# Performance work log

Hardware: AMD Instinct MI355X
Metric: run time of the kernel (lower is better)

## Reference

```python
import jax, jax.numpy as jnp
import numpy as np

EMBED_DIM = 1024
NUM_HEADS = 8                      # diff-attn heads; effective standard heads = 2*NUM_HEADS
HEAD_DIM = EMBED_DIM // NUM_HEADS // 2   # 64
DEPTH = 12
LAMBDA_INIT = 0.8 - 0.6 * float(np.exp(-0.3 * DEPTH))
RMS_EPS = 1e-5


def _rope_interleaved(x, cos, sin):
    # x: [B,S,H,D]; cos,sin: [S,D//2]. GPT-J style: rotate (even, odd) pairs.
    x1, x2 = x[..., ::2], x[..., 1::2]
    c = cos[None, :, None, :]
    s = sin[None, :, None, :]
    o1 = x1 * c - x2 * s
    o2 = x1 * s + x2 * c
    return jnp.stack([o1, o2], axis=-1).reshape(x.shape)


def _causal_attn(q, k, v, scale):
    # q,k: [B,S,H,D]; v: [B,S,H,Dv] -> out [B,S,H,Dv]
    S = q.shape[1]
    scores = jnp.einsum('bqhd,bkhd->bhqk', q, k) * scale
    causal = jnp.tril(jnp.ones((S, S), dtype=bool))
    scores = jnp.where(causal[None, None], scores, jnp.finfo(scores.dtype).min)
    p = jax.nn.softmax(scores, axis=-1)
    return jnp.einsum('bhqk,bkhd->bqhd', p, v)


def setup_inputs() -> dict:
    key = jax.random.key(0)
    ks = jax.random.split(key, 10)
    B, S, E, D = 1, 2048, EMBED_DIM, HEAD_DIM
    x = jax.random.normal(ks[0], (B, S, E), jnp.float32)
    # real rotary tables, rotary_dim = head_dim = 64 -> cos/sin [S, 32]
    inv_freq = 1.0 / (10000.0 ** (np.arange(0, D, 2, dtype=np.float64) / D))
    freqs = np.outer(np.arange(S, dtype=np.float64), inv_freq)
    cos = jnp.asarray(np.cos(freqs), jnp.float32)
    sin = jnp.asarray(np.sin(freqs), jnp.float32)
    sc = 1.0 / np.sqrt(E)
    wq = jax.random.normal(ks[1], (E, E), jnp.float32) * sc
    wk = jax.random.normal(ks[2], (E, E), jnp.float32) * sc
    wv = jax.random.normal(ks[3], (E, E), jnp.float32) * sc
    wo = jax.random.normal(ks[4], (E, E), jnp.float32) * sc
    lambda_q1 = jax.random.normal(ks[5], (D,), jnp.float32) * 0.1
    lambda_k1 = jax.random.normal(ks[6], (D,), jnp.float32) * 0.1
    lambda_q2 = jax.random.normal(ks[7], (D,), jnp.float32) * 0.1
    lambda_k2 = jax.random.normal(ks[8], (D,), jnp.float32) * 0.1
    subln_weight = jnp.ones((2 * D,), jnp.float32)
    return dict(x=x, cos=cos, sin=sin, wq=wq, wk=wk, wv=wv, wo=wo,
                lambda_q1=lambda_q1, lambda_k1=lambda_k1,
                lambda_q2=lambda_q2, lambda_k2=lambda_k2,
                subln_weight=subln_weight)


def reference(x, cos, sin, wq, wk, wv, wo,
              lambda_q1, lambda_k1, lambda_q2, lambda_k2, subln_weight):
    B, S, E = x.shape
    H, D = NUM_HEADS, HEAD_DIM
    q = (x @ wq).reshape(B, S, 2 * H, D)
    k = (x @ wk).reshape(B, S, 2 * H, D)
    v = (x @ wv).reshape(B, S, H, 2 * D)
    q = _rope_interleaved(q, cos, sin)
    k = _rope_interleaved(k, cos, sin)
    q = q.reshape(B, S, H, 2, D)
    k = k.reshape(B, S, H, 2, D)
    q1, q2 = q[..., 0, :], q[..., 1, :]
    k1, k2 = k[..., 0, :], k[..., 1, :]
    scale = D ** -0.5  # flash_attn default softmax scale
    a1 = _causal_attn(q1, k1, v, scale)  # [B,S,H,2D]
    a2 = _causal_attn(q2, k2, v, scale)
    lam1 = jnp.exp(jnp.sum(lambda_q1 * lambda_k1))
    lam2 = jnp.exp(jnp.sum(lambda_q2 * lambda_k2))
    lam_full = lam1 - lam2 + LAMBDA_INIT
    attn = a1 - lam_full * a2
    # sublayer RMSNorm over 2*head_dim, computed in fp32
    ms = jnp.mean(jnp.square(attn.astype(jnp.float32)), axis=-1, keepdims=True)
    attn = (attn.astype(jnp.float32) * jax.lax.rsqrt(ms + RMS_EPS)).astype(attn.dtype)
    attn = attn * subln_weight
    attn = attn * (1.0 - LAMBDA_INIT)
    attn = attn.reshape(B, S, E)
    return attn @ wo
```

## Files before the change

kernel.cpp:

```cpp
#include <hip/hip_runtime.h>
#include <hip/hip_bf16.h>

#define SEQ 2048
#define EMB 1024
#define NH 8
#define HD 64
#define DVH 128
#define LAMBDA_INIT 0.7836057665316245f
#define ONE_MINUS_LI 0.2163942334683755f
#define RMS_EPS 1e-5f
#define QK_SCALE 0.18033688011112042f

typedef __attribute__((ext_vector_type(8))) short short8_t;
typedef __attribute__((ext_vector_type(4))) float f32x4;

__device__ __forceinline__ short f2bf(float f) {
    __hip_bfloat16 h = __float2bfloat16(f);
    return *reinterpret_cast<short*>(&h);
}
__device__ __forceinline__ float bf2f(short s) {
    unsigned u = ((unsigned)(unsigned short)s) << 16;
    return __uint_as_float(u);
}
__device__ __forceinline__ float fast_exp2(float x) {
    float r;
    asm("v_exp_f32 %0, %1" : "=v"(r) : "v"(x));
    return r;
}
__device__ __forceinline__ void gload16(const void* g, void* l) {
    __builtin_amdgcn_global_load_lds((const __attribute__((address_space(1))) unsigned int*)g,
                                     (__attribute__((address_space(3))) unsigned int*)l, 16, 0, 0);
}

__global__ __launch_bounds__(256) void k_prep(const float* __restrict__ x, short* __restrict__ xb,
                                              const float* __restrict__ w0, const float* __restrict__ w1,
                                              const float* __restrict__ w2, const float* __restrict__ w3,
                                              short* __restrict__ o0, short* __restrict__ o1,
                                              short* __restrict__ o2, short* __restrict__ o3,
                                              const float* __restrict__ lq1, const float* __restrict__ lk1,
                                              const float* __restrict__ lq2, const float* __restrict__ lk2,
                                              float* __restrict__ lam) {
    const int bid = blockIdx.x;
    const int tid = threadIdx.x;
    if (bid < 2048) {
        int i = bid * 256 + tid;
        const float4* xv = (const float4*)x;
        float4 v = xv[i];
        short4 r = make_short4(f2bf(v.x), f2bf(v.y), f2bf(v.z), f2bf(v.w));
        *(short4*)(xb + i * 4) = r;
    } else if (bid < 3072) {
        int t = bid - 2048;
        int bz = t >> 8, by = (t >> 4) & 15, bx = t & 15;
        const float* w = bz == 0 ? w0 : bz == 1 ? w1 : bz == 2 ? w2 : w3;
        short* o = bz == 0 ? o0 : bz == 1 ? o1 : bz == 2 ? o2 : o3;
        __shared__ float tbuf[64][65];
        int r0 = by * 64, c0 = bx * 64;
        int col = tid & 63, rb = tid >> 6;
#pragma unroll
        for (int i = 0; i < 16; i++) {
            int row = rb + i * 4;
            tbuf[row][col] = w[(r0 + row) * EMB + c0 + col];
        }
        __syncthreads();
#pragma unroll
        for (int i = 0; i < 16; i++) {
            int fr = rb + i * 4;
            o[(c0 + fr) * EMB + r0 + col] = f2bf(tbuf[col][fr]);
        }
    } else {
        if (tid < 64) {
            float p1 = lq1[tid] * lk1[tid], p2 = lq2[tid] * lk2[tid];
#pragma unroll
            for (int off = 32; off >= 1; off >>= 1) {
                p1 += __shfl_xor(p1, off);
                p2 += __shfl_xor(p2, off);
            }
            if (tid == 0) lam[0] = expf(p1) - expf(p2) + LAMBDA_INIT;
        }
    }
}

template <int MI, int NI, int OUTM>
__global__ __launch_bounds__(256) void k_gemm(const short* __restrict__ A,
                                              const short* __restrict__ B0,
                                              const short* __restrict__ B1,
                                              const short* __restrict__ B2,
                                              const float* __restrict__ cosT,
                                              const float* __restrict__ sinT,
                                              short* __restrict__ Cq, short* __restrict__ Ktl,
                                              short* __restrict__ Vtl, float* __restrict__ Cf) {
    constexpr int BM = MI * 32, BN = NI * 32, BK = 64;
    constexpr int STAGE_SZ = (BM + BN) * BK;
    constexpr int SH_EPI = (OUTM == 0) ? BM * 136 : 0;
    constexpr int SHSZ = (2 * STAGE_SZ > SH_EPI) ? 2 * STAGE_SZ : SH_EPI;
    __shared__ short SH[SHSZ];
    const int bn = blockIdx.x * BN;
    const int bm = blockIdx.y * BM;
    const int nsel = bn >> 10;
    const int nloc = bn & 1023;
    const short* Bt = nsel == 0 ? B0 : (nsel == 1 ? B1 : B2);
    const int tid = threadIdx.x;
    const int w = tid >> 6, l = tid & 63;
    const int lr = l & 15, lg = l >> 4;
    const int wm = (w >> 1) * (MI * 16), wn = (w & 1) * (NI * 16);
    const int lrow8 = l >> 3, lchunk = l & 7;
    const int schunk = (lchunk ^ lrow8) * 8;

    f32x4 acc[MI][NI];
#pragma unroll
    for (int mi = 0; mi < MI; mi++)
#pragma unroll
        for (int ni = 0; ni < NI; ni++) acc[mi][ni] = f32x4{0.f, 0.f, 0.f, 0.f};

#define STAGEIT(BUF, K0)                                                                      \
    {                                                                                         \
        short* Ab_ = SH + (BUF) * STAGE_SZ;                                                   \
        short* Bb_ = Ab_ + BM * BK;                                                           \
        _Pragma("unroll") for (int j = 0; j < BM / 32; j++) {                                 \
            int r0 = w * (BM / 4) + j * 8;                                                    \
            gload16(A + (size_t)(bm + r0 + lrow8) * EMB + (K0) + schunk, &Ab_[r0 * BK]);      \
        }                                                                                     \
        _Pragma("unroll") for (int j = 0; j < BN / 32; j++) {                                 \
            int r0 = w * (BN / 4) + j * 8;                                                    \
            gload16(Bt + (size_t)(nloc + r0 + lrow8) * EMB + (K0) + schunk, &Bb_[r0 * BK]);   \
        }                                                                                     \
    }

    STAGEIT(0, 0);
    __syncthreads();
#pragma unroll 1
    for (int t = 0; t < EMB / BK; ++t) {
        const int cur = t & 1;
        if (t + 1 < EMB / BK) STAGEIT(cur ^ 1, (t + 1) * BK);
        const short* Ab_ = SH + cur * STAGE_SZ;
        const short* Bb_ = Ab_ + BM * BK;
#pragma unroll
        for (int kk = 0; kk < 2; kk++) {
            const int pcs = (((kk << 2) + lg) ^ (lr & 7)) << 3;
            short8_t af[MI], bf[NI];
#pragma unroll
            for (int mi = 0; mi < MI; mi++)
                af[mi] = *(const short8_t*)&Ab_[(wm + mi * 16 + lr) * BK + pcs];
#pragma unroll
            for (int ni = 0; ni < NI; ni++)
                bf[ni] = *(const short8_t*)&Bb_[(wn + ni * 16 + lr) * BK + pcs];
#pragma unroll
            for (int mi = 0; mi < MI; mi++)
#pragma unroll
                for (int ni = 0; ni < NI; ni++)
                    acc[mi][ni] =
                        __builtin_amdgcn_mfma_f32_16x16x32_bf16(af[mi], bf[ni], acc[mi][ni], 0, 0, 0);
        }
        __syncthreads();
    }
#undef STAGEIT

    if (OUTM == 1) {
#pragma unroll
        for (int mi = 0; mi < MI; mi++)
#pragma unroll
            for (int ni = 0; ni < NI; ni++)
#pragma unroll
                for (int r = 0; r < 4; r++) {
                    int row = bm + wm + mi * 16 + lg * 4 + r;
                    int col = wn + ni * 16 + lr;
                    Cf[row * EMB + bn + col] = acc[mi][ni][r];
                }
        return;
    }
    const int hh = nloc >> 7;
    short* tile = SH;
    if (nsel < 2) {
#pragma unroll
        for (int mi = 0; mi < MI; mi++)
#pragma unroll
            for (int ni = 0; ni < NI; ni++) {
                const int c = wn + ni * 16 + lr;
                const int p = (c & 63) >> 1;
#pragma unroll
                for (int r = 0; r < 4; r++) {
                    const int row = wm + mi * 16 + lg * 4 + r;
                    const int grow = bm + row;
                    float v = acc[mi][ni][r];
                    float partner = __shfl_xor(v, 1);
                    float cs = cosT[grow * 32 + p], sn = sinT[grow * 32 + p];
                    float out = (lr & 1) ? (partner * sn + v * cs) : (v * cs - partner * sn);
                    if (nsel == 0)
                        Cq[((size_t)hh << 18) + (size_t)grow * 128 + c] = f2bf(out * QK_SCALE);
                    else
                        tile[row * 136 + c] = f2bf(out);
                }
            }
        if (nsel == 1) {
            __syncthreads();
            const int kb0 = blockIdx.y * (BM / 32);
#pragma unroll
            for (int i = 0; i < BM / 16; i++) {
                int flat = tid + i * 256;
                int kbi = flat >> 9, rest = flat & 511;
                int slot = rest >> 6, ln = rest & 63;
                int lqq = ln & 15;
                int comp = slot >> 2, tt = (slot >> 1) & 1, s = slot & 1;
                int lgg = ln >> 4;
                int row = kbi * 32 + tt * 16 + lqq;
                int fb = comp * 64 + s * 32 + lgg * 8;
                short8_t v = *(const short8_t*)&tile[row * 136 + fb];
                *(short8_t*)(Ktl + ((size_t)(hh * 64 + kb0 + kbi) * 8 + slot) * 512 + ln * 8) = v;
            }
        }
    } else {
#pragma unroll
        for (int mi = 0; mi < MI; mi++)
#pragma unroll
            for (int ni = 0; ni < NI; ni++) {
                const int c = wn + ni * 16 + lr;
#pragma unroll
                for (int r = 0; r < 4; r++) {
                    const int row = wm + mi * 16 + lg * 4 + r;
                    tile[row * 136 + c] = f2bf(acc[mi][ni][r]);
                }
            }
        __syncthreads();
        const int kb0 = blockIdx.y * (BM / 32);
#pragma unroll
        for (int i = 0; i < BM / 16; i++) {
            int flat = tid + i * 256;
            int kbi = flat >> 9, rest = flat & 511;
            int dt = rest >> 6, ln = rest & 63;
            int lgg = ln >> 4, lqq = ln & 15;
            short8_t v;
#pragma unroll
            for (int j = 0; j < 8; j++)
                v[j] = tile[(kbi * 32 + 16 * (j >> 2) + 4 * lgg + (j & 3)) * 136 + dt * 16 + lqq];
            *(short8_t*)(Vtl + ((size_t)(hh * 64 + kb0 + kbi) * 8 + dt) * 512 + ln * 8) = v;
        }
    }
}

__global__ __launch_bounds__(512, 2) void k_attn(const short* __restrict__ Qh,
                                                 const short* __restrict__ Ktl,
                                                 const short* __restrict__ Vtl,
                                                 const float* __restrict__ lamp,
                                                 const float* __restrict__ subln,
                                                 short* __restrict__ Ab) {
    const int bid = blockIdx.x;
    const int h = bid & 7;
    const int ta = bid >> 3;
    const int tb = 63 - ta;
    const int q0a = ta * 32, q0b = tb * 32;
    const int nba = ta + 1, nbb = tb + 1;
    const int tid = threadIdx.x;
    const int w = tid >> 6, l = tid & 63;
    const int lq = l & 15, lg = l >> 4;
    const int comp = w >> 2, ks = w & 3;

    __shared__ __align__(16) float buf[2][2][16][132];
    __shared__ float LBp[2][4][16];

    short8_t qa0[2], qa1[2], qb0[2], qb1[2];
    {
        const short* qpa = Qh + ((size_t)h << 18) + (size_t)(q0a + lq) * 128 + (comp << 6) + lg * 8;
        qa0[0] = *(const short8_t*)(qpa);
        qa0[1] = *(const short8_t*)(qpa + 32);
        qa1[0] = *(const short8_t*)(qpa + 16 * 128);
        qa1[1] = *(const short8_t*)(qpa + 16 * 128 + 32);
        const short* qpb = Qh + ((size_t)h << 18) + (size_t)(q0b + lq) * 128 + (comp << 6) + lg * 8;
        qb0[0] = *(const short8_t*)(qpb);
        qb0[1] = *(const short8_t*)(qpb + 32);
        qb1[0] = *(const short8_t*)(qpb + 16 * 128);
        qb1[1] = *(const short8_t*)(qpb + 16 * 128 + 32);
    }
    f32x4 zero4 = {0.f, 0.f, 0.f, 0.f};
    f32x4 oa0[8], oa1[8], ob0[8], ob1[8];
#pragma unroll
    for (int dt = 0; dt < 8; dt++) {
        oa0[dt] = zero4;
        oa1[dt] = zero4;
        ob0[dt] = zero4;
        ob1[dt] = zero4;
    }
    float lsa0 = 0.f, lsa1 = 0.f, lsb0 = 0.f, lsb1 = 0.f;

    short8_t vf[8];
    short8_t kf[2][2];

#define PROC1(O, LS, QF, QROW, K0P)                                                          \
    {                                                                                        \
        f32x4 s_[2];                                                                         \
        s_[0] = zero4;                                                                       \
        s_[0] = __builtin_amdgcn_mfma_f32_16x16x32_bf16(kf[0][0], QF[0], s_[0], 0, 0, 0);    \
        s_[0] = __builtin_amdgcn_mfma_f32_16x16x32_bf16(kf[0][1], QF[1], s_[0], 0, 0, 0);    \
        s_[1] = zero4;                                                                       \
        s_[1] = __builtin_amdgcn_mfma_f32_16x16x32_bf16(kf[1][0], QF[0], s_[1], 0, 0, 0);    \
        s_[1] = __builtin_amdgcn_mfma_f32_16x16x32_bf16(kf[1][1], QF[1], s_[1], 0, 0, 0);    \
        float p_[8];                                                                         \
        _Pragma("unroll") for (int tt = 0; tt < 2; tt++)                                     \
            _Pragma("unroll") for (int r = 0; r < 4; r++) p_[tt * 4 + r] = s_[tt][r];        \
        if ((K0P) + 31 > (QROW)) {                                                           \
            _Pragma("unroll") for (int tt = 0; tt < 2; tt++)                                 \
                _Pragma("unroll") for (int r = 0; r < 4; r++) {                              \
                    int kk = (K0P) + tt * 16 + lg * 4 + r;                                   \
                    if (kk > (QROW) + lq) p_[tt * 4 + r] = -1e30f;                           \
                }                                                                            \
        }                                                                                    \
        _Pragma("unroll") for (int i = 0; i < 8; i++) {                                      \
            p_[i] = fast_exp2(p_[i]);                                                        \
            LS += p_[i];                                                                     \
        }                                                                                    \
        unsigned pu_[4];                                                                     \
        _Pragma("unroll") for (int pr = 0; pr < 4; pr++) {                                   \
            float2 f_ = {p_[2 * pr], p_[2 * pr + 1]};                                        \
            __hip_bfloat162 h_ = __float22bfloat162_rn(f_);                                  \
            __builtin_memcpy(&pu_[pr], &h_, 4);                                              \
        }                                                                                    \
        short8_t pa_;                                                                        \
        __builtin_memcpy(&pa_, pu_, 16);                                                     \
        _Pragma("unroll") for (int dt = 0; dt < 8; dt++)                                     \
            O[dt] = __builtin_amdgcn_mfma_f32_16x16x32_bf16(pa_, vf[dt], O[dt], 0, 0, 0);    \
    }

#pragma unroll 1
    for (int kb = ks; kb < nbb; kb += 4) {
        const int k0p = kb * 32;
        {
            const short* vtb = Vtl + (size_t)(h * 64 + kb) * 4096 + l * 8;
            const short* ktb = Ktl + ((size_t)(h * 64 + kb) * 8 + comp * 4) * 512 + l * 8;
#pragma unroll
            for (int dt = 0; dt < 8; dt++) vf[dt] = *(const short8_t*)(vtb + dt * 512);
#pragma unroll
            for (int tt = 0; tt < 2; tt++) {
                kf[tt][0] = *(const short8_t*)(ktb + (tt * 2) * 512);
                kf[tt][1] = *(const short8_t*)(ktb + (tt * 2 + 1) * 512);
            }
        }
        PROC1(ob0, lsb0, qb0, q0b, k0p);
        PROC1(ob1, lsb1, qb1, q0b + 16, k0p);
        if (kb < nba) {
            PROC1(oa0, lsa0, qa0, q0a, k0p);
            PROC1(oa1, lsa1, qa1, q0a + 16, k0p);
        }
    }
#undef PROC1

    lsa0 += __shfl_xor(lsa0, 16);
    lsa0 += __shfl_xor(lsa0, 32);
    lsa1 += __shfl_xor(lsa1, 16);
    lsa1 += __shfl_xor(lsa1, 32);
    lsb0 += __shfl_xor(lsb0, 16);
    lsb0 += __shfl_xor(lsb0, 32);
    lsb1 += __shfl_xor(lsb1, 16);
    lsb1 += __shfl_xor(lsb1, 32);

#define MERGE(O, LS, QBASE)                                                                  \
    {                                                                                        \
        if (ks >= 2) {                                                                       \
            _Pragma("unroll") for (int dt = 0; dt < 8; dt++)                                 \
                _Pragma("unroll") for (int r = 0; r < 4; r++)                                \
                    buf[comp][ks - 2][lg * 4 + r][dt * 16 + lq] = O[dt][r];                  \
            if (l < 16) LBp[comp][ks][l] = LS;                                               \
        }                                                                                    \
        __syncthreads();                                                                     \
        f32x4 oacc_[8];                                                                      \
        float lacc_ = LS;                                                                    \
        if (ks < 2) {                                                                        \
            _Pragma("unroll") for (int dt = 0; dt < 8; dt++)                                 \
                _Pragma("unroll") for (int r = 0; r < 4; r++)                                \
                    oacc_[dt][r] = O[dt][r] + buf[comp][ks][lg * 4 + r][dt * 16 + lq];       \
            lacc_ = LS + LBp[comp][ks + 2][lq];                                              \
        }                                                                                    \
        __syncthreads();                                                                     \
        if (ks == 1) {                                                                       \
            _Pragma("unroll") for (int dt = 0; dt < 8; dt++)                                 \
                _Pragma("unroll") for (int r = 0; r < 4; r++)                                \
                    buf[comp][0][lg * 4 + r][dt * 16 + lq] = oacc_[dt][r];                   \
            if (l < 16) LBp[comp][1][l] = lacc_;                                             \
        }                                                                                    \
        __syncthreads();                                                                     \
        if (ks == 0) {                                                                       \
            _Pragma("unroll") for (int dt = 0; dt < 8; dt++)                                 \
                _Pragma("unroll") for (int r = 0; r < 4; r++)                                \
                    oacc_[dt][r] += buf[comp][0][lg * 4 + r][dt * 16 + lq];                  \
            lacc_ += LBp[comp][1][lq];                                                       \
            const float cs_ = comp ? lamp[0] : 1.f;                                         \
            float inv_[4];                                                                   \
            _Pragma("unroll") for (int r = 0; r < 4; r++)                                    \
                inv_[r] = cs_ / __shfl(lacc_, lg * 4 + r);                                   \
            _Pragma("unroll") for (int dt = 0; dt < 8; dt++)                                 \
                _Pragma("unroll") for (int r = 0; r < 4; r++)                                \
                    buf[comp][1][lg * 4 + r][dt * 16 + lq] = oacc_[dt][r] * inv_[r];         \
        }                                                                                    \
        __syncthreads();                                                                     \
        if (tid < 128) {                                                                     \
            const int row_ = tid >> 3;                                                       \
            const int c0_ = (tid & 7) * 16;                                                  \
            float a_[16], ss_ = 0.f;                                                         \
            _Pragma("unroll") for (int j = 0; j < 16; j++) {                                 \
                a_[j] = buf[0][1][row_][c0_ + j] - buf[1][1][row_][c0_ + j];                 \
                ss_ += a_[j] * a_[j];                                                        \
            }                                                                                \
            ss_ += __shfl_xor(ss_, 1);                                                       \
            ss_ += __shfl_xor(ss_, 2);                                                       \
            ss_ += __shfl_xor(ss_, 4);                                                       \
            const float sc_ = rsqrtf(ss_ * (1.0f / 128.0f) + RMS_EPS) * ONE_MINUS_LI;        \
            short8_t r8_;                                                                    \
            _Pragma("unroll") for (int j = 0; j < 8; j++)                                    \
                r8_[j] = f2bf(a_[j] * sc_ * subln[c0_ + j]);                                 \
            *(short8_t*)(Ab + (size_t)((QBASE) + row_) * EMB + h * DVH + c0_) = r8_;         \
            _Pragma("unroll") for (int j = 0; j < 8; j++)                                    \
                r8_[j] = f2bf(a_[8 + j] * sc_ * subln[c0_ + 8 + j]);                         \
            *(short8_t*)(Ab + (size_t)((QBASE) + row_) * EMB + h * DVH + c0_ + 8) = r8_;     \
        }                                                                                    \
        __syncthreads();                                                                     \
    }

    MERGE(ob0, lsb0, q0b);
    MERGE(ob1, lsb1, q0b + 16);
    MERGE(oa0, lsa0, q0a);
    MERGE(oa1, lsa1, q0a + 16);
#undef MERGE
}

extern "C" void kernel_launch(void* const* d_in, const int* in_sizes, int n_in,
                              void* d_out, int out_size, void* d_ws, size_t ws_size,
                              hipStream_t stream) {
    const float* x = (const float*)d_in[0];
    const float* cosT = (const float*)d_in[1];
    const float* sinT = (const float*)d_in[2];
    const float* wq = (const float*)d_in[3];
    const float* wk = (const float*)d_in[4];
    const float* wv = (const float*)d_in[5];
    const float* wo = (const float*)d_in[6];
    const float* lq1 = (const float*)d_in[7];
    const float* lk1 = (const float*)d_in[8];
    const float* lq2 = (const float*)d_in[9];
    const float* lk2 = (const float*)d_in[10];
    const float* subln = (const float*)d_in[11];
    float* out = (float*)d_out;
    char* ws = (char*)d_ws;
    const size_t MB = 1 << 20;
    short* xb = (short*)(ws);
    short* wqt = (short*)(ws + 4 * MB);
    short* wkt = (short*)(ws + 6 * MB);
    short* wvt = (short*)(ws + 8 * MB);
    short* wot = (short*)(ws + 10 * MB);
    short* Qh = (short*)(ws + 12 * MB);
    short* Vtl = (short*)(ws + 20 * MB);
    short* Ktl = (short*)(ws + 24 * MB);
    short* Ab = (short*)(ws + 28 * MB);
    float* lam = (float*)(ws + 32 * MB);

    k_prep<<<3073, 256, 0, stream>>>(x, xb, wq, wk, wv, wo, wqt, wkt, wvt, wot, lq1, lk1, lq2,
                                     lk2, lam);
    k_gemm<2, 4, 0><<<dim3(24, 32), 256, 0, stream>>>(xb, wqt, wkt, wvt, cosT, sinT, Qh, Ktl,
                                                      Vtl, nullptr);
    k_attn<<<256, 512, 0, stream>>>(Qh, Ktl, Vtl, lam, subln, Ab);
    k_gemm<2, 2, 1><<<dim3(16, 32), 256, 0, stream>>>(Ab, wot, wot, wot, nullptr, nullptr,
                                                      nullptr, nullptr, nullptr, out);
}
```

Baseline: 77.58 us.

## Halve attention block to two K-split waves and double-buffer K/V loads

The attention kernel drops from 8 waves (4-way key split per component) to 4 waves (2-way split), each wave walking its key blocks with ping-pong register buffers so the next block's K/V loads are issued before the current block's MFMAs. The cross-wave merge shrinks from a two-stage reduction with three barriers to a single store/sync/add. In exchange, each block has half the waves to hide latency, more registers per thread (launch bounds 256,1), and each wave does twice the serial work per block.

```diff
diff --git a/kernel.cpp b/kernel.cpp
--- a/kernel.cpp
+++ b/kernel.cpp
@@ -237,7 +237,7 @@
     }
 }
 
-__global__ __launch_bounds__(512, 2) void k_attn(const short* __restrict__ Qh,
+__global__ __launch_bounds__(256, 1) void k_attn(const short* __restrict__ Qh,
                                                  const short* __restrict__ Ktl,
                                                  const short* __restrict__ Vtl,
                                                  const float* __restrict__ lamp,
@@ -252,10 +252,10 @@
     const int tid = threadIdx.x;
     const int w = tid >> 6, l = tid & 63;
     const int lq = l & 15, lg = l >> 4;
-    const int comp = w >> 2, ks = w & 3;
+    const int comp = w >> 1, ks = w & 1;
 
     __shared__ __align__(16) float buf[2][2][16][132];
-    __shared__ float LBp[2][4][16];
+    __shared__ float LBp[2][16];
 
     short8_t qa0[2], qa1[2], qb0[2], qb1[2];
     {
@@ -281,18 +281,30 @@
     }
     float lsa0 = 0.f, lsa1 = 0.f, lsb0 = 0.f, lsb1 = 0.f;
 
-    short8_t vf[8];
-    short8_t kf[2][2];
-
-#define PROC1(O, LS, QF, QROW, K0P)                                                          \
+    short8_t vfA[8], vfB[8];
+    short8_t kfA[2][2], kfB[2][2];
+
+#define LOADKV(VF, KF, KB)                                                                  \
+    {                                                                                       \
+        const short* vtb = Vtl + (size_t)(h * 64 + (KB)) * 4096 + l * 8;                    \
+        const short* ktb = Ktl + ((size_t)(h * 64 + (KB)) * 8 + comp * 4) * 512 + l * 8;    \
+        _Pragma("unroll") for (int dt = 0; dt < 8; dt++) VF[dt] =                           \
+            *(const short8_t*)(vtb + dt * 512);                                             \
+        _Pragma("unroll") for (int tt = 0; tt < 2; tt++) {                                  \
+            KF[tt][0] = *(const short8_t*)(ktb + (tt * 2) * 512);                           \
+            KF[tt][1] = *(const short8_t*)(ktb + (tt * 2 + 1) * 512);                       \
+        }                                                                                   \
+    }
+
+#define PROC1(O, LS, QF, QROW, K0P, KF, VF)                                                  \
     {                                                                                        \
         f32x4 s_[2];                                                                         \
         s_[0] = zero4;                                                                       \
-        s_[0] = __builtin_amdgcn_mfma_f32_16x16x32_bf16(kf[0][0], QF[0], s_[0], 0, 0, 0);    \
-        s_[0] = __builtin_amdgcn_mfma_f32_16x16x32_bf16(kf[0][1], QF[1], s_[0], 0, 0, 0);    \
+        s_[0] = __builtin_amdgcn_mfma_f32_16x16x32_bf16(KF[0][0], QF[0], s_[0], 0, 0, 0);    \
+        s_[0] = __builtin_amdgcn_mfma_f32_16x16x32_bf16(KF[0][1], QF[1], s_[0], 0, 0, 0);    \
         s_[1] = zero4;                                                                       \
-        s_[1] = __builtin_amdgcn_mfma_f32_16x16x32_bf16(kf[1][0], QF[0], s_[1], 0, 0, 0);    \
-        s_[1] = __builtin_amdgcn_mfma_f32_16x16x32_bf16(kf[1][1], QF[1], s_[1], 0, 0, 0);    \
+        s_[1] = __builtin_amdgcn_mfma_f32_16x16x32_bf16(KF[1][0], QF[0], s_[1], 0, 0, 0);    \
+        s_[1] = __builtin_amdgcn_mfma_f32_16x16x32_bf16(KF[1][1], QF[1], s_[1], 0, 0, 0);    \
         float p_[8];                                                                         \
         _Pragma("unroll") for (int tt = 0; tt < 2; tt++)                                     \
             _Pragma("unroll") for (int r = 0; r < 4; r++) p_[tt * 4 + r] = s_[tt][r];        \
@@ -316,31 +328,34 @@
         short8_t pa_;                                                                        \
         __builtin_memcpy(&pa_, pu_, 16);                                                     \
         _Pragma("unroll") for (int dt = 0; dt < 8; dt++)                                     \
-            O[dt] = __builtin_amdgcn_mfma_f32_16x16x32_bf16(pa_, vf[dt], O[dt], 0, 0, 0);    \
-    }
-
+            O[dt] = __builtin_amdgcn_mfma_f32_16x16x32_bf16(pa_, VF[dt], O[dt], 0, 0, 0);    \
+    }
+
+#define PROC4(KF, VF, KB)                                                                    \
+    {                                                                                        \
+        const int k0p_ = (KB) * 32;                                                          \
+        PROC1(ob0, lsb0, qb0, q0b, k0p_, KF, VF);                                            \
+        PROC1(ob1, lsb1, qb1, q0b + 16, k0p_, KF, VF);                                       \
+        if ((KB) < nba) {                                                                    \
+            PROC1(oa0, lsa0, qa0, q0a, k0p_, KF, VF);                                        \
+            PROC1(oa1, lsa1, qa1, q0a + 16, k0p_, KF, VF);                                   \
+        }                                                                                    \
+    }
+
+    LOADKV(vfA, kfA, ks);
 #pragma unroll 1
     for (int kb = ks; kb < nbb; kb += 4) {
-        const int k0p = kb * 32;
-        {
-            const short* vtb = Vtl + (size_t)(h * 64 + kb) * 4096 + l * 8;
-            const short* ktb = Ktl + ((size_t)(h * 64 + kb) * 8 + comp * 4) * 512 + l * 8;
-#pragma unroll
-            for (int dt = 0; dt < 8; dt++) vf[dt] = *(const short8_t*)(vtb + dt * 512);
-#pragma unroll
-            for (int tt = 0; tt < 2; tt++) {
-                kf[tt][0] = *(const short8_t*)(ktb + (tt * 2) * 512);
-                kf[tt][1] = *(const short8_t*)(ktb + (tt * 2 + 1) * 512);
-            }
-        }
-        PROC1(ob0, lsb0, qb0, q0b, k0p);
-        PROC1(ob1, lsb1, qb1, q0b + 16, k0p);
-        if (kb < nba) {
-            PROC1(oa0, lsa0, qa0, q0a, k0p);
-            PROC1(oa1, lsa1, qa1, q0a + 16, k0p);
-        }
-    }
+        const bool hb = (kb + 2) < nbb;
+        if (hb) LOADKV(vfB, kfB, kb + 2);
+        PROC4(kfA, vfA, kb);
+        if (hb) {
+            if (kb + 4 < nbb) LOADKV(vfA, kfA, kb + 4);
+            PROC4(kfB, vfB, kb + 2);
+        }
+    }
+#undef PROC4
 #undef PROC1
+#undef LOADKV
 
     lsa0 += __shfl_xor(lsa0, 16);
     lsa0 += __shfl_xor(lsa0, 32);
@@ -353,35 +368,20 @@
 
 #define MERGE(O, LS, QBASE)                                                                  \
     {                                                                                        \
-        if (ks >= 2) {                                                                       \
-            _Pragma("unroll") for (int dt = 0; dt < 8; dt++)                                 \
-                _Pragma("unroll") for (int r = 0; r < 4; r++)                                \
-                    buf[comp][ks - 2][lg * 4 + r][dt * 16 + lq] = O[dt][r];                  \
-            if (l < 16) LBp[comp][ks][l] = LS;                                               \
-        }                                                                                    \
-        __syncthreads();                                                                     \
-        f32x4 oacc_[8];                                                                      \
-        float lacc_ = LS;                                                                    \
-        if (ks < 2) {                                                                        \
-            _Pragma("unroll") for (int dt = 0; dt < 8; dt++)                                 \
-                _Pragma("unroll") for (int r = 0; r < 4; r++)                                \
-                    oacc_[dt][r] = O[dt][r] + buf[comp][ks][lg * 4 + r][dt * 16 + lq];       \
-            lacc_ = LS + LBp[comp][ks + 2][lq];                                              \
-        }                                                                                    \
-        __syncthreads();                                                                     \
         if (ks == 1) {                                                                       \
             _Pragma("unroll") for (int dt = 0; dt < 8; dt++)                                 \
                 _Pragma("unroll") for (int r = 0; r < 4; r++)                                \
-                    buf[comp][0][lg * 4 + r][dt * 16 + lq] = oacc_[dt][r];                   \
-            if (l < 16) LBp[comp][1][l] = lacc_;                                             \
+                    buf[comp][0][lg * 4 + r][dt * 16 + lq] = O[dt][r];                       \
+            if (l < 16) LBp[comp][l] = LS;                                                   \
         }                                                                                    \
         __syncthreads();                                                                     \
         if (ks == 0) {                                                                       \
+            f32x4 oacc_[8];                                                                  \
             _Pragma("unroll") for (int dt = 0; dt < 8; dt++)                                 \
                 _Pragma("unroll") for (int r = 0; r < 4; r++)                                \
-                    oacc_[dt][r] += buf[comp][0][lg * 4 + r][dt * 16 + lq];                  \
-            lacc_ += LBp[comp][1][lq];                                                       \
-            const float cs_ = comp ? lamp[0] : 1.f;                                         \
+                    oacc_[dt][r] = O[dt][r] + buf[comp][0][lg * 4 + r][dt * 16 + lq];        \
+            float lacc_ = LS + LBp[comp][lq];                                                \
+            const float cs_ = comp ? lamp[0] : 1.f;                                          \
             float inv_[4];                                                                   \
             _Pragma("unroll") for (int r = 0; r < 4; r++)                                    \
                 inv_[r] = cs_ / __shfl(lacc_, lg * 4 + r);                                   \
@@ -453,7 +453,7 @@
                                      lk2, lam);
     k_gemm<2, 4, 0><<<dim3(24, 32), 256, 0, stream>>>(xb, wqt, wkt, wvt, cosT, sinT, Qh, Ktl,
                                                       Vtl, nullptr);
-    k_attn<<<256, 512, 0, stream>>>(Qh, Ktl, Vtl, lam, subln, Ab);
+    k_attn<<<256, 256, 0, stream>>>(Qh, Ktl, Vtl, lam, subln, Ab);
     k_gemm<2, 2, 1><<<dim3(16, 32), 256, 0, stream>>>(Ab, wot, wot, wot, nullptr, nullptr,
                                                       nullptr, nullptr, nullptr, out);
 }
```

After: 82.14 us. 5.9% more time.
